# Performance work log

Measured on AMD Instinct MI355X. Metric: run time of the kernel, lower is better.

Reference implementation:

```python
import jax, jax.numpy as jnp
import numpy as np

HEADS = 16

def setup_inputs() -> dict:
    key = jax.random.key(0)
    k1, k2, k3 = jax.random.split(key, 3)
    B, S, D = 4, 2048, 1024
    x = jax.random.normal(k1, (B, S, D), dtype=jnp.float32)
    w_qkv = jax.random.normal(k2, (D, 3 * D), dtype=jnp.float32) * (D ** -0.5)
    w_out = jax.random.normal(k3, (D, D), dtype=jnp.float32) * (D ** -0.5)
    return {"x": x, "w_qkv": w_qkv, "w_out": w_out}

def reference(x, w_qkv, w_out):
    B, S, D = x.shape
    H = HEADS
    hd = D // H
    qkv = jnp.einsum("bsd,de->bse", x, w_qkv)  # [B,S,3D]
    q, k, v = jnp.split(qkv, 3, axis=-1)
    # [B,S,D] -> [B,H,S,hd]
    q = q.reshape(B, S, H, hd).transpose(0, 2, 1, 3)
    k = k.reshape(B, S, H, hd).transpose(0, 2, 1, 3)
    v = v.reshape(B, S, H, hd).transpose(0, 2, 1, 3)
    scores = jnp.einsum("bhqd,bhkd->bhqk", q, k) / jnp.sqrt(jnp.float32(hd))
    attn = jax.nn.softmax(scores, axis=-1)
    out = jnp.einsum("bhqk,bhkd->bhqd", attn, v)  # [B,H,S,hd]
    out = out.transpose(0, 2, 1, 3).reshape(B, S, D)
    return jnp.einsum("bsd,de->bse", out, w_out)
```

## Files before the change

kernel.cpp:

```cpp
#include <hip/hip_runtime.h>

typedef __bf16 bf16;
typedef __bf16 bfx8 __attribute__((ext_vector_type(8)));
typedef __bf16 bfx4 __attribute__((ext_vector_type(4)));
typedef float f32x4 __attribute__((ext_vector_type(4)));

#define MFMA_BF16 __builtin_amdgcn_mfma_f32_16x16x32_bf16

static constexpr int Bq = 4, Sq = 2048, Dq = 1024, Hq = 16, HDq = 64;
static constexpr int Mq = Bq * Sq;
static constexpr int D3 = 3 * Dq;
static constexpr int NQK = 2 * Dq;
static constexpr float L2E = 1.4426950408889634f;
static constexpr float QSC = 0.125f * L2E;

typedef const __attribute__((address_space(1))) void* gas1;
typedef __attribute__((address_space(3))) void* las3;

__device__ __forceinline__ void gload_lds16(const bf16* g, bf16* l) {
    __builtin_amdgcn_global_load_lds((gas1)g, (las3)l, 16, 0, 0);
}

__device__ __forceinline__ float fast_exp2(float x) {
    return __builtin_amdgcn_exp2f(x);
}

__global__ __launch_bounds__(256) void cast_f32_bf16(const float* __restrict__ in,
                                                     bf16* __restrict__ out, int n) {
    int i = (blockIdx.x * 256 + threadIdx.x) * 4;
    if (i + 3 < n) {
        float4 v = *(const float4*)(in + i);
        bfx4 r;
        r[0] = (bf16)v.x; r[1] = (bf16)v.y; r[2] = (bf16)v.z; r[3] = (bf16)v.w;
        *(bfx4*)(out + i) = r;
    }
}

__global__ __launch_bounds__(256) void transpose_cast(const float* __restrict__ in,
                                                      bf16* __restrict__ out, int R, int C) {
    __shared__ float tile[32][33];
    int tx = threadIdx.x, ty = threadIdx.y;
    int c0 = blockIdx.x * 32, r0 = blockIdx.y * 32;
    for (int j = 0; j < 32; j += 8)
        tile[ty + j][tx] = in[(size_t)(r0 + ty + j) * C + c0 + tx];
    __syncthreads();
    for (int j = 0; j < 32; j += 8)
        out[(size_t)(c0 + ty + j) * R + r0 + tx] = (bf16)tile[tx][ty + j];
}

template <bool OUT_F32, bool QSCALE, bool VSPLIT>
__global__ __launch_bounds__(256) void gemm_bt(const bf16* __restrict__ A,
                                               const bf16* __restrict__ Bt,
                                               void* __restrict__ Cout,
                                               bf16* __restrict__ Vout,
                                               int M, int N, int K) {
    __shared__ bf16 As[128 * 64];
    __shared__ bf16 Bs[128 * 64];
    int m0 = blockIdx.y * 128;
    int n0 = blockIdx.x * 128;
    int tid = threadIdx.x;
    int lane = tid & 63, wave = tid >> 6;
    int quad = lane >> 4, l16 = lane & 15;
    int wr = wave >> 1, wc = wave & 1;
    int sw = l16 & 7;

    f32x4 acc[4][4] = {};

    for (int k0 = 0; k0 < K; k0 += 64) {
        __syncthreads();
        #pragma unroll
        for (int i = 0; i < 4; i++) {
            int c = i * 256 + tid;
            int row = c >> 3;
            int ch = (c & 7) ^ (row & 7);
            gload_lds16(A + (size_t)(m0 + row) * K + k0 + ch * 8, As + c * 8);
            gload_lds16(Bt + (size_t)(n0 + row) * K + k0 + ch * 8, Bs + c * 8);
        }
        __syncthreads();
        #pragma unroll
        for (int s = 0; s < 2; s++) {
            bfx8 af[4], bfr[4];
            #pragma unroll
            for (int i = 0; i < 4; i++)
                af[i] = *(const bfx8*)(As + (wr * 64 + i * 16 + l16) * 64 +
                                       ((s * 4 + quad) ^ sw) * 8);
            #pragma unroll
            for (int j = 0; j < 4; j++)
                bfr[j] = *(const bfx8*)(Bs + (wc * 64 + j * 16 + l16) * 64 +
                                        ((s * 4 + quad) ^ sw) * 8);
            #pragma unroll
            for (int i = 0; i < 4; i++)
                #pragma unroll
                for (int j = 0; j < 4; j++)
                    acc[i][j] = MFMA_BF16(af[i], bfr[j], acc[i][j], 0, 0, 0);
        }
    }

    #pragma unroll
    for (int i = 0; i < 4; i++)
        #pragma unroll
        for (int j = 0; j < 4; j++) {
            int col = n0 + wc * 64 + j * 16 + l16;
            if (VSPLIT && col >= NQK) {
                int d = col - NQK;
                int row0 = m0 + wr * 64 + i * 16 + quad * 4;
                int b = row0 >> 11, s0 = row0 & (Sq - 1);
                int w = s0 & 63;
                int sp = (s0 & ~63) | (((w >> 5) * 4 + ((w >> 2) & 3)) * 8) |
                         (((w >> 4) & 1) * 4);
                bfx4 pv;
                #pragma unroll
                for (int r = 0; r < 4; r++) pv[r] = (bf16)acc[i][j][r];
                *(bfx4*)(Vout + ((size_t)b * Dq + d) * Sq + sp) = pv;
            } else {
                int cstride = VSPLIT ? NQK : N;
                float scale = (QSCALE && col < Dq) ? QSC : 1.0f;
                #pragma unroll
                for (int r = 0; r < 4; r++) {
                    int row = m0 + wr * 64 + i * 16 + quad * 4 + r;
                    if (OUT_F32)
                        ((float*)Cout)[(size_t)row * cstride + col] = acc[i][j][r];
                    else
                        ((bf16*)Cout)[(size_t)row * cstride + col] = (bf16)(acc[i][j][r] * scale);
                }
            }
        }
}

__global__ __launch_bounds__(256, 4) void attn_kernel(const bf16* __restrict__ qkv,
                                                      const bf16* __restrict__ Vt,
                                                      bf16* __restrict__ out) {
    __shared__ bf16 Ks[2][64 * 64];
    __shared__ bf16 Vs[2][64 * 64];

    int bid = blockIdx.x;
    int qc = (bid >> 3) & 15;
    int head = ((bid >> 7) << 3) | (bid & 7);
    int h = head & 15, b = head >> 4;
    int tid = threadIdx.x;
    int lane = tid & 63, wave = tid >> 6;
    int quad = lane >> 4, l16 = lane & 15;
    int sw = l16 & 7;

    size_t base = (size_t)b * Sq * NQK;
    const bf16* Kbase = qkv + base + Dq + h * HDq;
    const bf16* Vbase = Vt + ((size_t)b * Dq + h * HDq) * Sq;
    int q0 = qc * 128 + wave * 32;

    bfx8 qf[2][2];
    #pragma unroll
    for (int qt = 0; qt < 2; qt++)
        #pragma unroll
        for (int s = 0; s < 2; s++)
            qf[qt][s] = *(const bfx8*)(qkv + base + (size_t)(q0 + qt * 16 + l16) * NQK +
                                       h * HDq + s * 32 + quad * 8);

    bfx8 ones;
    #pragma unroll
    for (int j = 0; j < 8; j++) ones[j] = (bf16)1.0f;

    f32x4 oacc[2][4] = {};
    f32x4 lacc[2] = {};

    int c0 = tid, c1 = tid + 256;
    int r0 = c0 >> 3, ch0 = (c0 & 7) ^ (r0 & 7);
    int r1 = c1 >> 3, ch1 = (c1 & 7) ^ (r1 & 7);

    gload_lds16(Kbase + (size_t)r0 * NQK + ch0 * 8, Ks[0] + c0 * 8);
    gload_lds16(Vbase + (size_t)r0 * Sq + ch0 * 8, Vs[0] + c0 * 8);
    gload_lds16(Kbase + (size_t)r1 * NQK + ch1 * 8, Ks[0] + c1 * 8);
    gload_lds16(Vbase + (size_t)r1 * Sq + ch1 * 8, Vs[0] + c1 * 8);

    for (int i = 0; i < 32; i++) {
        int cur = i & 1;
        __syncthreads();
        if (i + 1 < 32) {
            int k0 = (i + 1) * 64;
            bf16* kd = Ks[cur ^ 1];
            bf16* vd = Vs[cur ^ 1];
            gload_lds16(Kbase + (size_t)(k0 + r0) * NQK + ch0 * 8, kd + c0 * 8);
            gload_lds16(Vbase + (size_t)r0 * Sq + k0 + ch0 * 8, vd + c0 * 8);
            gload_lds16(Kbase + (size_t)(k0 + r1) * NQK + ch1 * 8, kd + c1 * 8);
            gload_lds16(Vbase + (size_t)r1 * Sq + k0 + ch1 * 8, vd + c1 * 8);
        }
        const bf16* K_ = Ks[cur];
        const bf16* V_ = Vs[cur];

        #pragma unroll
        for (int hf = 0; hf < 2; hf++) {
            bfx8 kf[2][2];
            #pragma unroll
            for (int tp = 0; tp < 2; tp++) {
                int krow = ((2 * hf + tp) * 16 + l16) * 64;
                kf[tp][0] = *(const bfx8*)(K_ + krow + (quad ^ sw) * 8);
                kf[tp][1] = *(const bfx8*)(K_ + krow + ((4 + quad) ^ sw) * 8);
            }

            bfx8 pf[2];
            #pragma unroll
            for (int qt = 0; qt < 2; qt++) {
                f32x4 s0 = {}, s1 = {};
                s0 = MFMA_BF16(kf[0][0], qf[qt][0], s0, 0, 0, 0);
                s0 = MFMA_BF16(kf[0][1], qf[qt][1], s0, 0, 0, 0);
                s1 = MFMA_BF16(kf[1][0], qf[qt][0], s1, 0, 0, 0);
                s1 = MFMA_BF16(kf[1][1], qf[qt][1], s1, 0, 0, 0);
                bfx8 p;
                #pragma unroll
                for (int r = 0; r < 4; r++) {
                    p[r]     = (bf16)fast_exp2(s0[r]);
                    p[4 + r] = (bf16)fast_exp2(s1[r]);
                }
                pf[qt] = p;
                lacc[qt] = MFMA_BF16(pf[qt], ones, lacc[qt], 0, 0, 0);
            }

            #pragma unroll
            for (int nt = 0; nt < 4; nt++) {
                bfx8 vf = *(const bfx8*)(V_ + (nt * 16 + l16) * 64 +
                                         ((hf * 4 + quad) ^ sw) * 8);
                #pragma unroll
                for (int qt = 0; qt < 2; qt++)
                    oacc[qt][nt] = MFMA_BF16(pf[qt], vf, oacc[qt][nt], 0, 0, 0);
            }
        }
    }

    #pragma unroll
    for (int qt = 0; qt < 2; qt++)
        #pragma unroll
        for (int r = 0; r < 4; r++) {
            int row = q0 + qt * 16 + quad * 4 + r;
            float inv = 1.0f / lacc[qt][r];
            #pragma unroll
            for (int nt = 0; nt < 4; nt++)
                out[((size_t)b * Sq + row) * Dq + h * HDq + nt * 16 + l16] =
                    (bf16)(oacc[qt][nt][r] * inv);
        }
}

extern "C" void kernel_launch(void* const* d_in, const int* in_sizes, int n_in,
                              void* d_out, int out_size, void* d_ws, size_t ws_size,
                              hipStream_t stream) {
    const float* x     = (const float*)d_in[0];
    const float* w_qkv = (const float*)d_in[1];
    const float* w_out = (const float*)d_in[2];
    float* out = (float*)d_out;

    char* ws = (char*)d_ws;
    bf16* x_bf   = (bf16*)ws;
    bf16* wqkvT  = (bf16*)(ws + 16777216);
    bf16* woutT  = (bf16*)(ws + 16777216 + 6291456);
    bf16* qkv2   = (bf16*)(ws + 25165824);
    bf16* Vt     = (bf16*)(ws + 25165824 + 33554432);
    bf16* attn   = x_bf;

    cast_f32_bf16<<<(Mq * Dq) / 4 / 256, 256, 0, stream>>>(x, x_bf, Mq * Dq);
    dim3 tb(32, 8);
    transpose_cast<<<dim3(D3 / 32, Dq / 32), tb, 0, stream>>>(w_qkv, wqkvT, Dq, D3);
    transpose_cast<<<dim3(Dq / 32, Dq / 32), tb, 0, stream>>>(w_out, woutT, Dq, Dq);

    gemm_bt<false, true, true><<<dim3(D3 / 128, Mq / 128), 256, 0, stream>>>(
        x_bf, wqkvT, qkv2, Vt, Mq, D3, Dq);

    attn_kernel<<<1024, 256, 0, stream>>>(qkv2, Vt, attn);

    gemm_bt<true, false, false><<<dim3(Dq / 128, Mq / 128), 256, 0, stream>>>(
        attn, woutT, out, nullptr, Mq, Dq, Dq);
}
```

Measured before the change: 257.8 us.

## Use double-buffered 256x256 QKV GEMM, block swizzle, and MFMA priority hints

Replaces the QKV projection GEMM with a 512-thread kernel that computes 256x256 output tiles. It double-buffers the LDS staging with explicit vmcnt waits and interleaves LDS fragment loads with MFMA quadrants under s_setprio. The output-projection GEMM gains an XCD-aware block-index swizzle, and the attention kernel regroups its MFMAs under raised wave priority. The aim is to hide global-load latency, raise data reuse per tile and improve L2 locality. The cost is higher register and LDS pressure (128 KB LDS per block) and lower occupancy.

```diff
diff --git a/kernel.cpp b/kernel.cpp
--- a/kernel.cpp
+++ b/kernel.cpp
@@ -48,62 +48,113 @@
         out[(size_t)(c0 + ty + j) * R + r0 + tx] = (bf16)tile[tx][ty + j];
 }
 
-template <bool OUT_F32, bool QSCALE, bool VSPLIT>
-__global__ __launch_bounds__(256) void gemm_bt(const bf16* __restrict__ A,
-                                               const bf16* __restrict__ Bt,
-                                               void* __restrict__ Cout,
-                                               bf16* __restrict__ Vout,
-                                               int M, int N, int K) {
-    __shared__ bf16 As[128 * 64];
-    __shared__ bf16 Bs[128 * 64];
-    int m0 = blockIdx.y * 128;
-    int n0 = blockIdx.x * 128;
+template <int MQ>
+__device__ __forceinline__ void lda256(bfx8 (&af)[4][2], const bf16* Ah,
+                                       int l16, int quad, int sw) {
+    #pragma unroll
+    for (int i = 0; i < 4; i++)
+        #pragma unroll
+        for (int s = 0; s < 2; s++)
+            af[i][s] = *(const bfx8*)(Ah + (MQ * 64 + i * 16 + l16) * 64 +
+                                      (((s * 4 + quad) ^ sw) * 8));
+}
+template <int NQ>
+__device__ __forceinline__ void ldb256(bfx8 (&bfr)[2][2], const bf16* Bh, int wc1,
+                                       int l16, int quad, int sw) {
+    #pragma unroll
+    for (int j = 0; j < 2; j++)
+        #pragma unroll
+        for (int s = 0; s < 2; s++)
+            bfr[j][s] = *(const bfx8*)(Bh + (wc1 * 64 + (NQ * 2 + j) * 16 + l16) * 64 +
+                                       (((s * 4 + quad) ^ sw) * 8));
+}
+template <int MQ, int NQ>
+__device__ __forceinline__ void mma256(f32x4 (&acc)[8][4], const bfx8 (&af)[4][2],
+                                       const bfx8 (&bfr)[2][2]) {
+    #pragma unroll
+    for (int s = 0; s < 2; s++)
+        #pragma unroll
+        for (int i = 0; i < 4; i++)
+            #pragma unroll
+            for (int j = 0; j < 2; j++)
+                acc[MQ * 4 + i][NQ * 2 + j] =
+                    MFMA_BF16(af[i][s], bfr[j][s], acc[MQ * 4 + i][NQ * 2 + j], 0, 0, 0);
+}
+
+__device__ __forceinline__ void stage256(const bf16* A, const bf16* Bt, int K,
+                                         bf16* Asd, bf16* Bsd, int m0, int n0,
+                                         int k0, int tid) {
+    #pragma unroll
+    for (int L = 0; L < 2; L++) {
+        int c = L * 512 + tid;
+        int row = c >> 3;
+        int ch = (c & 7) ^ (row & 7);
+        gload_lds16(A + (size_t)(m0 + row) * K + k0 + ch * 8, Asd + c * 8);
+        gload_lds16(A + (size_t)(m0 + 128 + row) * K + k0 + ch * 8, Asd + 8192 + c * 8);
+        gload_lds16(Bt + (size_t)(n0 + row) * K + k0 + ch * 8, Bsd + c * 8);
+        gload_lds16(Bt + (size_t)(n0 + 128 + row) * K + k0 + ch * 8, Bsd + 8192 + c * 8);
+    }
+}
+
+__global__ __launch_bounds__(512, 2) void gemm256_qkv(const bf16* __restrict__ A,
+                                                      const bf16* __restrict__ Bt,
+                                                      bf16* __restrict__ Cqk,
+                                                      bf16* __restrict__ Vout) {
+    __shared__ bf16 As[2][2 * 8192];
+    __shared__ bf16 Bs[2][2 * 8192];
+    constexpr int K = Dq, NBX = D3 / 256, NWG = NBX * (Mq / 256);
+    int bid = blockIdx.x;
+    int swz = (bid & 7) * (NWG >> 3) + (bid >> 3);
+    int n0 = (swz % NBX) * 256;
+    int m0 = (swz / NBX) * 256;
     int tid = threadIdx.x;
     int lane = tid & 63, wave = tid >> 6;
     int quad = lane >> 4, l16 = lane & 15;
-    int wr = wave >> 1, wc = wave & 1;
+    int wr = wave >> 2, wc = wave & 3;
+    int wc1 = wc & 1;
     int sw = l16 & 7;
 
-    f32x4 acc[4][4] = {};
-
-    for (int k0 = 0; k0 < K; k0 += 64) {
-        __syncthreads();
-        #pragma unroll
-        for (int i = 0; i < 4; i++) {
-            int c = i * 256 + tid;
-            int row = c >> 3;
-            int ch = (c & 7) ^ (row & 7);
-            gload_lds16(A + (size_t)(m0 + row) * K + k0 + ch * 8, As + c * 8);
-            gload_lds16(Bt + (size_t)(n0 + row) * K + k0 + ch * 8, Bs + c * 8);
-        }
-        __syncthreads();
-        #pragma unroll
-        for (int s = 0; s < 2; s++) {
-            bfx8 af[4], bfr[4];
-            #pragma unroll
-            for (int i = 0; i < 4; i++)
-                af[i] = *(const bfx8*)(As + (wr * 64 + i * 16 + l16) * 64 +
-                                       ((s * 4 + quad) ^ sw) * 8);
-            #pragma unroll
-            for (int j = 0; j < 4; j++)
-                bfr[j] = *(const bfx8*)(Bs + (wc * 64 + j * 16 + l16) * 64 +
-                                        ((s * 4 + quad) ^ sw) * 8);
-            #pragma unroll
-            for (int i = 0; i < 4; i++)
-                #pragma unroll
-                for (int j = 0; j < 4; j++)
-                    acc[i][j] = MFMA_BF16(af[i], bfr[j], acc[i][j], 0, 0, 0);
-        }
-    }
-
-    #pragma unroll
-    for (int i = 0; i < 4; i++)
+    f32x4 acc[8][4] = {};
+
+    stage256(A, Bt, K, &As[0][0], &Bs[0][0], m0, n0, 0, tid);
+
+    #pragma unroll 1
+    for (int t = 0; t < 16; t++) {
+        if (t < 15) {
+            stage256(A, Bt, K, &As[(t + 1) & 1][0], &Bs[(t + 1) & 1][0],
+                     m0, n0, (t + 1) * 64, tid);
+            asm volatile("s_waitcnt vmcnt(8)" ::: "memory");
+        } else {
+            asm volatile("s_waitcnt vmcnt(0)" ::: "memory");
+        }
+        __builtin_amdgcn_s_barrier();
+        const bf16* Ah = &As[t & 1][wr * 8192];
+        const bf16* Bh = &Bs[t & 1][(wc >> 1) * 8192];
+        bfx8 af[4][2], bfr[2][2];
+        lda256<0>(af, Ah, l16, quad, sw);
+        ldb256<0>(bfr, Bh, wc1, l16, quad, sw);
+        __builtin_amdgcn_s_barrier();
+        __builtin_amdgcn_s_setprio(1); mma256<0, 0>(acc, af, bfr); __builtin_amdgcn_s_setprio(0);
+        ldb256<1>(bfr, Bh, wc1, l16, quad, sw);
+        __builtin_amdgcn_s_barrier();
+        __builtin_amdgcn_s_setprio(1); mma256<0, 1>(acc, af, bfr); __builtin_amdgcn_s_setprio(0);
+        lda256<1>(af, Ah, l16, quad, sw);
+        __builtin_amdgcn_s_barrier();
+        __builtin_amdgcn_s_setprio(1); mma256<1, 1>(acc, af, bfr); __builtin_amdgcn_s_setprio(0);
+        ldb256<0>(bfr, Bh, wc1, l16, quad, sw);
+        asm volatile("s_waitcnt lgkmcnt(0)" ::: "memory");
+        __builtin_amdgcn_s_barrier();
+        __builtin_amdgcn_s_setprio(1); mma256<1, 0>(acc, af, bfr); __builtin_amdgcn_s_setprio(0);
+    }
+
+    #pragma unroll
+    for (int i = 0; i < 8; i++)
         #pragma unroll
         for (int j = 0; j < 4; j++) {
             int col = n0 + wc * 64 + j * 16 + l16;
-            if (VSPLIT && col >= NQK) {
+            int row0 = m0 + wr * 128 + i * 16 + quad * 4;
+            if (col >= NQK) {
                 int d = col - NQK;
-                int row0 = m0 + wr * 64 + i * 16 + quad * 4;
                 int b = row0 >> 11, s0 = row0 & (Sq - 1);
                 int w = s0 & 63;
                 int sp = (s0 & ~63) | (((w >> 5) * 4 + ((w >> 2) & 3)) * 8) |
@@ -113,16 +164,76 @@
                 for (int r = 0; r < 4; r++) pv[r] = (bf16)acc[i][j][r];
                 *(bfx4*)(Vout + ((size_t)b * Dq + d) * Sq + sp) = pv;
             } else {
-                int cstride = VSPLIT ? NQK : N;
-                float scale = (QSCALE && col < Dq) ? QSC : 1.0f;
+                float scale = (col < Dq) ? QSC : 1.0f;
                 #pragma unroll
-                for (int r = 0; r < 4; r++) {
-                    int row = m0 + wr * 64 + i * 16 + quad * 4 + r;
-                    if (OUT_F32)
-                        ((float*)Cout)[(size_t)row * cstride + col] = acc[i][j][r];
-                    else
-                        ((bf16*)Cout)[(size_t)row * cstride + col] = (bf16)(acc[i][j][r] * scale);
-                }
+                for (int r = 0; r < 4; r++)
+                    Cqk[(size_t)(row0 + r) * NQK + col] = (bf16)(acc[i][j][r] * scale);
+            }
+        }
+}
+
+template <bool OUT_F32>
+__global__ __launch_bounds__(256) void gemm_bt(const bf16* __restrict__ A,
+                                               const bf16* __restrict__ Bt,
+                                               void* __restrict__ Cout,
+                                               int M, int N, int K) {
+    __shared__ bf16 As[128 * 64];
+    __shared__ bf16 Bs[128 * 64];
+    int nwg = gridDim.x * gridDim.y;
+    int lin = blockIdx.y * gridDim.x + blockIdx.x;
+    int swzb = (lin & 7) * (nwg >> 3) + (lin >> 3);
+    int m0 = (swzb / gridDim.x) * 128;
+    int n0 = (swzb % gridDim.x) * 128;
+    int tid = threadIdx.x;
+    int lane = tid & 63, wave = tid >> 6;
+    int quad = lane >> 4, l16 = lane & 15;
+    int wr = wave >> 1, wc = wave & 1;
+    int sw = l16 & 7;
+
+    f32x4 acc[4][4] = {};
+
+    for (int k0 = 0; k0 < K; k0 += 64) {
+        __syncthreads();
+        #pragma unroll
+        for (int i = 0; i < 4; i++) {
+            int c = i * 256 + tid;
+            int row = c >> 3;
+            int ch = (c & 7) ^ (row & 7);
+            gload_lds16(A + (size_t)(m0 + row) * K + k0 + ch * 8, As + c * 8);
+            gload_lds16(Bt + (size_t)(n0 + row) * K + k0 + ch * 8, Bs + c * 8);
+        }
+        __syncthreads();
+        #pragma unroll
+        for (int s = 0; s < 2; s++) {
+            bfx8 af[4], bfr[4];
+            #pragma unroll
+            for (int i = 0; i < 4; i++)
+                af[i] = *(const bfx8*)(As + (wr * 64 + i * 16 + l16) * 64 +
+                                       ((s * 4 + quad) ^ sw) * 8);
+            #pragma unroll
+            for (int j = 0; j < 4; j++)
+                bfr[j] = *(const bfx8*)(Bs + (wc * 64 + j * 16 + l16) * 64 +
+                                        ((s * 4 + quad) ^ sw) * 8);
+            #pragma unroll
+            for (int i = 0; i < 4; i++)
+                #pragma unroll
+                for (int j = 0; j < 4; j++)
+                    acc[i][j] = MFMA_BF16(af[i], bfr[j], acc[i][j], 0, 0, 0);
+        }
+    }
+
+    #pragma unroll
+    for (int i = 0; i < 4; i++)
+        #pragma unroll
+        for (int j = 0; j < 4; j++) {
+            int col = n0 + wc * 64 + j * 16 + l16;
+            #pragma unroll
+            for (int r = 0; r < 4; r++) {
+                int row = m0 + wr * 64 + i * 16 + quad * 4 + r;
+                if (OUT_F32)
+                    ((float*)Cout)[(size_t)row * N + col] = acc[i][j][r];
+                else
+                    ((bf16*)Cout)[(size_t)row * N + col] = (bf16)acc[i][j][r];
             }
         }
 }
@@ -200,10 +311,12 @@
             #pragma unroll
             for (int qt = 0; qt < 2; qt++) {
                 f32x4 s0 = {}, s1 = {};
+                __builtin_amdgcn_s_setprio(1);
                 s0 = MFMA_BF16(kf[0][0], qf[qt][0], s0, 0, 0, 0);
                 s0 = MFMA_BF16(kf[0][1], qf[qt][1], s0, 0, 0, 0);
                 s1 = MFMA_BF16(kf[1][0], qf[qt][0], s1, 0, 0, 0);
                 s1 = MFMA_BF16(kf[1][1], qf[qt][1], s1, 0, 0, 0);
+                __builtin_amdgcn_s_setprio(0);
                 bfx8 p;
                 #pragma unroll
                 for (int r = 0; r < 4; r++) {
@@ -211,17 +324,19 @@
                     p[4 + r] = (bf16)fast_exp2(s1[r]);
                 }
                 pf[qt] = p;
-                lacc[qt] = MFMA_BF16(pf[qt], ones, lacc[qt], 0, 0, 0);
-            }
-
+            }
+
+            __builtin_amdgcn_s_setprio(1);
+            lacc[0] = MFMA_BF16(pf[0], ones, lacc[0], 0, 0, 0);
+            lacc[1] = MFMA_BF16(pf[1], ones, lacc[1], 0, 0, 0);
             #pragma unroll
             for (int nt = 0; nt < 4; nt++) {
                 bfx8 vf = *(const bfx8*)(V_ + (nt * 16 + l16) * 64 +
                                          ((hf * 4 + quad) ^ sw) * 8);
-                #pragma unroll
-                for (int qt = 0; qt < 2; qt++)
-                    oacc[qt][nt] = MFMA_BF16(pf[qt], vf, oacc[qt][nt], 0, 0, 0);
-            }
+                oacc[0][nt] = MFMA_BF16(pf[0], vf, oacc[0][nt], 0, 0, 0);
+                oacc[1][nt] = MFMA_BF16(pf[1], vf, oacc[1][nt], 0, 0, 0);
+            }
+            __builtin_amdgcn_s_setprio(0);
         }
     }
 
@@ -259,11 +374,10 @@
     transpose_cast<<<dim3(D3 / 32, Dq / 32), tb, 0, stream>>>(w_qkv, wqkvT, Dq, D3);
     transpose_cast<<<dim3(Dq / 32, Dq / 32), tb, 0, stream>>>(w_out, woutT, Dq, Dq);
 
-    gemm_bt<false, true, true><<<dim3(D3 / 128, Mq / 128), 256, 0, stream>>>(
-        x_bf, wqkvT, qkv2, Vt, Mq, D3, Dq);
+    gemm256_qkv<<<384, 512, 0, stream>>>(x_bf, wqkvT, qkv2, Vt);
 
     attn_kernel<<<1024, 256, 0, stream>>>(qkv2, Vt, attn);
 
-    gemm_bt<true, false, false><<<dim3(Dq / 128, Mq / 128), 256, 0, stream>>>(
-        attn, woutT, out, nullptr, Mq, Dq, Dq);
-}
+    gemm_bt<true><<<dim3(Dq / 128, Mq / 128), 256, 0, stream>>>(
+        attn, woutT, out, Mq, Dq, Dq);
+}
```

Result: slower. 268.3 us (+4.1%).
